# Performance work log

Hardware: AMD Instinct MI355X
Metric: run time of the kernel (lower is better)

The kernel has to match this reference:

```python
import jax, jax.numpy as jnp
import numpy as np

K = 3            # snake kernel size
MORPH = 0        # extend along depth axis
EXT = 1.0        # extend_scope
EPS = 1e-5
GROUPS = 16      # out_planes // 4


def conv3d(x, w, b, stride=(1, 1, 1), padding='SAME'):
    out = jax.lax.conv_general_dilated(
        x, w, window_strides=stride, padding=padding,
        dimension_numbers=('NCDHW', 'OIDHW', 'NCDHW'))
    return out + b[None, :, None, None, None]


def batchnorm(x, g, b):
    # training-mode BatchNorm3d (batch statistics, biased variance)
    m = x.mean(axis=(0, 2, 3, 4), keepdims=True)
    v = x.var(axis=(0, 2, 3, 4), keepdims=True)
    return (x - m) / jnp.sqrt(v + EPS) * g[None, :, None, None, None] + b[None, :, None, None, None]


def groupnorm(x, g, b):
    B, C, D, H, W = x.shape
    xg = x.reshape(B, GROUPS, C // GROUPS, D, H, W)
    m = xg.mean(axis=(2, 3, 4, 5), keepdims=True)
    v = xg.var(axis=(2, 3, 4, 5), keepdims=True)
    xn = ((xg - m) / jnp.sqrt(v + EPS)).reshape(B, C, D, H, W)
    return xn * g[None, :, None, None, None] + b[None, :, None, None, None]


def cumulative_offsets(off):
    # off: [B, K, D, H, W]; accumulate outward from kernel center (snake chaining)
    center = K // 2
    cums = [None] * K
    cums[center] = jnp.zeros_like(off[:, 0])
    for i in range(1, center + 1):
        cums[center + i] = cums[center + i - 1] + off[:, center + i]
        cums[center - i] = cums[center - i + 1] + off[:, center - i]
    return jnp.stack(cums, axis=1)  # [B, K, D, H, W]


def trilinear_sample_one(feat, z, y, x):
    # feat: [C, D, H, W]; z/y/x: [DK, H, W] float coords (already clamped)
    C, D, H, W = feat.shape
    z0f, y0f, x0f = jnp.floor(z), jnp.floor(y), jnp.floor(x)
    wz, wy, wx = z - z0f, y - y0f, x - x0f
    z0 = jnp.clip(z0f.astype(jnp.int32), 0, D - 1)
    y0 = jnp.clip(y0f.astype(jnp.int32), 0, H - 1)
    x0 = jnp.clip(x0f.astype(jnp.int32), 0, W - 1)
    z1 = jnp.clip(z0 + 1, 0, D - 1)
    y1 = jnp.clip(y0 + 1, 0, H - 1)
    x1 = jnp.clip(x0 + 1, 0, W - 1)

    def g(zi, yi, xi):
        return feat[:, zi, yi, xi]  # [C, DK, H, W]

    out = (g(z0, y0, x0) * ((1 - wz) * (1 - wy) * (1 - wx))[None]
         + g(z0, y0, x1) * ((1 - wz) * (1 - wy) * wx)[None]
         + g(z0, y1, x0) * ((1 - wz) * wy * (1 - wx))[None]
         + g(z0, y1, x1) * ((1 - wz) * wy * wx)[None]
         + g(z1, y0, x0) * (wz * (1 - wy) * (1 - wx))[None]
         + g(z1, y0, x1) * (wz * (1 - wy) * wx)[None]
         + g(z1, y1, x0) * (wz * wy * (1 - wx))[None]
         + g(z1, y1, x1) * (wz * wy * wx)[None])
    return out


def setup_inputs() -> dict:
    key = jax.random.key(0)
    ks = jax.random.split(key, 8)
    B, Cin, Cout, D, H, W = 2, 32, 64, 48, 48, 48
    x = jax.random.normal(ks[0], (B, Cin, D, H, W), dtype=jnp.float32)
    offset_w = jax.random.normal(ks[1], (3 * K, Cin, 3, 3, 3), dtype=jnp.float32) * 0.02
    offset_b = jnp.zeros((3 * K,), dtype=jnp.float32)
    bn_g = jnp.ones((3 * K,), dtype=jnp.float32)
    bn_b = jnp.zeros((3 * K,), dtype=jnp.float32)
    conv_w = jax.random.normal(ks[2], (Cout, Cin, K, 1, 1), dtype=jnp.float32) * 0.05
    conv_b = jnp.zeros((Cout,), dtype=jnp.float32)
    gn_g = jnp.ones((Cout,), dtype=jnp.float32)
    gn_b = jnp.zeros((Cout,), dtype=jnp.float32)
    return {"x": x, "offset_w": offset_w, "offset_b": offset_b, "bn_g": bn_g,
            "bn_b": bn_b, "conv_w": conv_w, "conv_b": conv_b, "gn_g": gn_g, "gn_b": gn_b}


def reference(x, offset_w, offset_b, bn_g, bn_b, conv_w, conv_b, gn_g, gn_b):
    B, C, D, H, W = x.shape
    dt = x.dtype
    # offset prediction: tanh(BN(conv3x3x3)) -> [B, 3K, D, H, W]
    off = jnp.tanh(batchnorm(conv3d(x, offset_w, offset_b), bn_g, bn_b))
    off_y = off[:, K:2 * K]   # perpendicular offsets (morph=0: H and W)
    off_x = off[:, 2 * K:]
    cy = cumulative_offsets(off_y)  # [B, K, D, H, W]
    cx = cumulative_offsets(off_x)
    center = K // 2
    kk = jnp.arange(K, dtype=dt) - center
    # coordinate maps [B, K, D, H, W]
    z = jnp.broadcast_to(jnp.arange(D, dtype=dt)[None, None, :, None, None]
                         + kk[None, :, None, None, None], (B, K, D, H, W))
    y = jnp.arange(H, dtype=dt)[None, None, None, :, None] + EXT * cy
    xc = jnp.arange(W, dtype=dt)[None, None, None, None, :] + EXT * cx
    z = jnp.clip(z, 0.0, D - 1)
    y = jnp.clip(y, 0.0, H - 1)
    xc = jnp.clip(xc, 0.0, W - 1)
    # interleave kernel points along depth: [B, D*K, H, W]
    il = lambda c: jnp.transpose(c, (0, 2, 1, 3, 4)).reshape(B, D * K, H, W)
    z, y, xc = il(z), il(y), il(xc)
    deformed = jax.vmap(trilinear_sample_one)(x, z, y, xc)  # [B, C, D*K, H, W]
    out = conv3d(deformed, conv_w, conv_b, stride=(K, 1, 1), padding='VALID')
    return jax.nn.relu(groupnorm(out, gn_g, gn_b))
```

## Files before the change

kernel.cpp:

```cpp
#include <hip/hip_runtime.h>
#include <hip/hip_bf16.h>

#define ZB    2
#define ZCIN  32
#define ZCOUT 64
#define ZD    48
#define ZH    48
#define ZW    48
#define ZHW   2304
#define ZDHW  110592
#define ZNPOS 221184
#define ZEPS  1e-5f

#define WFLAG    0
#define WCB      64
#define WBNSTAT  128
#define WGNSTAT  192
#define WBMAT    256
#define WBMATO   3328
#define WCONV    10240
#define WXTP     894976


template <int TAG>
__device__ __forceinline__ float ldT(const void* p, long i) {
    if (TAG == 1) return __bfloat162float(((const __hip_bfloat16*)p)[i]);
    return ((const float*)p)[i];
}

__device__ __forceinline__ unsigned short f2bu(float f) {
    unsigned int b = __float_as_uint(f);
    b += 0x7FFFu + ((b >> 16) & 1u);
    return (unsigned short)(b >> 16);
}
__device__ __forceinline__ float bu2f(unsigned short u) {
    return __uint_as_float(((unsigned int)u) << 16);
}

typedef short bf16x8 __attribute__((ext_vector_type(8)));
typedef float f32x4  __attribute__((ext_vector_type(4)));
typedef unsigned short u16x8 __attribute__((ext_vector_type(8)));

template <int TAG>
__device__ void begin_prep(const void* offset_w, const void* conv_w,
                           const void* conv_b, float* ws, int i) {
    if (i < 64) {
        ws[WCB + i] = ldT<TAG>(conv_b, i);
    } else if (i < 6208) {
        int j = i - 64;
        int n = j / 96, kk = j % 96;
        int kz = kk >> 5, ci = kk & 31;
        ((unsigned short*)(ws + WBMAT))[j] =
            f2bu(ldT<TAG>(conv_w, ((long)n * 32 + ci) * 3 + kz));
    } else if (i < 20032) {
        int j = i - 6208;
        int tap = j / 512, rem = j % 512;
        int n = rem >> 5, ci = rem & 31;
        float v = 0.f;
        if (n < 4) {
            int ch = (n == 0) ? 3 : (n == 1) ? 5 : (n == 2) ? 6 : 8;
            v = ldT<TAG>(offset_w, (long)ch * 864 + ci * 27 + tap);
        }
        ((unsigned short*)(ws + WBMATO))[j] = f2bu(v);
    } else if (i < 20160) {
        ws[WBNSTAT + (i - 20032)] = 0.0f;
    }
}

__device__ void begin_zero_boundary(float* ws, int v) {
    if (v >= 28816) return;
    int b = v / 14408, r = v % 14408;
    int z, y, x;
    if (r < 5000) {
        z = (r / 2500) * 49; int q = r % 2500; y = q / 50; x = q % 50;
    } else if (r < 9800) {
        int s = r - 5000; z = 1 + s / 100; int q = s % 100;
        y = (q / 50) * 49; x = q % 50;
    } else {
        int s = r - 9800; z = 1 + s / 96; int q = s % 96;
        y = 1 + q / 2; x = (q & 1) * 49;
    }
    unsigned short* xtp = (unsigned short*)(ws + WXTP);
    long base = ((((long)b * 50 + z) * 50 + y) * 50 + x) * 32;
    u16x8 zz = {0, 0, 0, 0, 0, 0, 0, 0};
#pragma unroll
    for (int k = 0; k < 4; ++k) *(u16x8*)&xtp[base + k * 8] = zz;
}

template <int TAG>
__device__ void begin_xpose(const void* x, float* ws, int bid2,
                            unsigned short* tile) {
    int b = bid2 / 2304, rem = bid2 % 2304;
    int z = rem / 48, y = rem % 48;
    int t = threadIdx.x;
    long ibase = (long)b * ZCIN * ZDHW + (long)z * ZHW + (long)y * ZW;
    if (TAG == 1) {
        if (t < 192) {
            int ci = t / 6, cb = t % 6;
            u16x8 v = *(const u16x8*)((const unsigned short*)x
                                      + ibase + (long)ci * ZDHW + cb * 8);
#pragma unroll
            for (int e = 0; e < 8; ++e)
                tile[(cb * 8 + e) * 34 + ci] = (unsigned short)v[e];
        }
    } else {
#pragma unroll
        for (int kk = 0; kk < 2; ++kk) {
            int c = t + kk * 256;
            if (c < 384) {
                int ci = c / 12, cb = c % 12;
                float4 v = *(const float4*)((const float*)x
                                            + ibase + (long)ci * ZDHW + cb * 4);
                tile[(cb * 4 + 0) * 34 + ci] = f2bu(v.x);
                tile[(cb * 4 + 1) * 34 + ci] = f2bu(v.y);
                tile[(cb * 4 + 2) * 34 + ci] = f2bu(v.z);
                tile[(cb * 4 + 3) * 34 + ci] = f2bu(v.w);
            }
        }
    }
    __syncthreads();
    long obase16 = ((((long)b * 50 + z + 1) * 50 + y + 1) * 50 + 1) * 32;
    unsigned int* o32 = (unsigned int*)((unsigned short*)(ws + WXTP) + obase16);
#pragma unroll
    for (int k = 0; k < 3; ++k) {
        int e2 = k * 256 + t;
        int xx = e2 >> 4, c2 = (e2 & 15) * 2;
        o32[e2] = (unsigned int)tile[xx * 34 + c2]
                | ((unsigned int)tile[xx * 34 + c2 + 1] << 16);
    }
}

__global__ void __launch_bounds__(256) zk_begin(const void* x, const void* offset_w,
                                                const void* conv_w, const void* conv_b,
                                                const unsigned short* bng, float* ws) {
    __shared__ unsigned short tile[48 * 34];
    int bid = blockIdx.x;
    bool isbf = (bng[0] != 0);
    if (bid < 79) {
        int i = bid * 256 + threadIdx.x;
        if (i == 0) ws[WFLAG] = isbf ? 1.0f : 2.0f;
        if (isbf) begin_prep<1>(offset_w, conv_w, conv_b, ws, i);
        else      begin_prep<2>(offset_w, conv_w, conv_b, ws, i);
    } else if (bid < 192) {
        begin_zero_boundary(ws, (bid - 79) * 256 + threadIdx.x);
    } else {
        if (isbf) begin_xpose<1>(x, ws, bid - 192, tile);
        else      begin_xpose<2>(x, ws, bid - 192, tile);
    }
}

__global__ void __launch_bounds__(256, 4) zk_offset_conv(float* ws) {
    const unsigned short* bmo = (const unsigned short*)(ws + WBMATO);
    const unsigned short* xtp = (const unsigned short*)(ws + WXTP);
    float* convout = ws + WCONV;

    __shared__ __align__(16) unsigned short slice[1280 * 8];
    __shared__ float sred[8];

    int t = threadIdx.x, lane = t & 63, wv = t >> 6;
    int quad = lane >> 4, col = lane & 15;
    int bid2 = (blockIdx.x & 7) * 144 + (blockIdx.x >> 3);
    int b  = bid2 / 576, rem = bid2 % 576;
    int z  = rem / 12, yt = rem % 12;
    int y0 = yt * 4;

    if (t < 8) sred[t] = 0.f;

    f32x4 acc[3];
#pragma unroll
    for (int mt = 0; mt < 3; ++mt) {
        acc[mt][0] = 0.f; acc[mt][1] = 0.f; acc[mt][2] = 0.f; acc[mt][3] = 0.f;
    }

#pragma unroll
    for (int kz = 0; kz < 3; ++kz) {
        long cb = (((long)b * 50 + (z + kz)) * 50 + y0) * 50 * 4;
        __syncthreads();
#pragma unroll
        for (int i = 0; i < 5; ++i) {
            int c = i * 256 + t;
            *(u16x8*)&slice[c * 8] = *(const u16x8*)&xtp[(cb + c) * 8];
        }
        __syncthreads();

        bf16x8 bfr[9];
#pragma unroll
        for (int j = 0; j < 9; ++j)
            bfr[j] = *(const bf16x8*)&bmo[((kz * 9 + j) * 16 + col) * 32 + quad * 8];

#pragma unroll
        for (int ky = 0; ky < 3; ++ky)
#pragma unroll
            for (int kx = 0; kx < 3; ++kx) {
                int j = ky * 3 + kx;
#pragma unroll
                for (int mt = 0; mt < 3; ++mt) {
                    int ch = ((wv + ky) * 50 + mt * 16 + col + kx) * 4 + quad;
                    bf16x8 a = *(const bf16x8*)&slice[ch * 8];
                    acc[mt] = __builtin_amdgcn_mfma_f32_16x16x32_bf16(
                                  a, bfr[j], acc[mt], 0, 0, 0);
                }
            }
    }

    float S = 0.f, Q = 0.f;
#pragma unroll
    for (int mt = 0; mt < 3; ++mt) {
        S += acc[mt][0] + acc[mt][1] + acc[mt][2] + acc[mt][3];
        Q += acc[mt][0] * acc[mt][0] + acc[mt][1] * acc[mt][1]
           + acc[mt][2] * acc[mt][2] + acc[mt][3] * acc[mt][3];
    }
    S += __shfl_xor(S, 16); S += __shfl_xor(S, 32);
    Q += __shfl_xor(Q, 16); Q += __shfl_xor(Q, 32);

    if (col < 4) {
        int rowbase = b * ZDHW + z * ZHW + (y0 + wv) * 48 + quad * 4;
#pragma unroll
        for (int mt = 0; mt < 3; ++mt)
            *(f32x4*)&convout[col * ZNPOS + rowbase + mt * 16] = acc[mt];
        if (quad == 0) {
            atomicAdd(&sred[col], S);
            atomicAdd(&sred[4 + col], Q);
        }
    }
    __syncthreads();
    if (t < 8) atomicAdd(&ws[WBNSTAT + t], sred[t]);
}

__device__ __forceinline__ void sample_plane(const unsigned short* xt,
        unsigned short* As, int tp, int kzslot, int b, int zp, int h, int w,
        float cy, float cx) {
    float fy = fminf(fmaxf((float)h + cy, 0.f), 47.f);
    float fx = fminf(fmaxf((float)w + cx, 0.f), 47.f);
    int y0 = (int)fy, x0 = (int)fx;
    float wy = fy - (float)y0, wx = fx - (float)x0;
    int y1 = (y0 < 47) ? y0 + 1 : 47, x1 = (x0 < 47) ? x0 + 1 : 47;
    long pb = ((long)b * 50 + zp + 1) * 50;
    long r0 = (pb + y0 + 1) * 50, r1 = (pb + y1 + 1) * 50;
    long a00 = (r0 + x0 + 1) * 32, a01 = (r0 + x1 + 1) * 32;
    long a10 = (r1 + x0 + 1) * 32, a11 = (r1 + x1 + 1) * 32;
    float u00 = (1.f - wy) * (1.f - wx), u01 = (1.f - wy) * wx;
    float u10 = wy * (1.f - wx),         u11 = wy * wx;
    u16x8 A[4], B[4], C[4], D[4];
#pragma unroll
    for (int j = 0; j < 4; ++j) {
        A[j] = *(const u16x8*)&xt[a00 + j * 8];
        B[j] = *(const u16x8*)&xt[a01 + j * 8];
        C[j] = *(const u16x8*)&xt[a10 + j * 8];
        D[j] = *(const u16x8*)&xt[a11 + j * 8];
    }
#pragma unroll
    for (int j = 0; j < 4; ++j) {
        u16x8 o;
#pragma unroll
        for (int e = 0; e < 8; ++e) {
            float v = u00 * bu2f((unsigned short)A[j][e])
                    + u01 * bu2f((unsigned short)B[j][e])
                    + u10 * bu2f((unsigned short)C[j][e])
                    + u11 * bu2f((unsigned short)D[j][e]);
            o[e] = f2bu(v);
        }
        *(u16x8*)&As[tp * 104 + kzslot * 32 + j * 8] = o;
    }
}

template <int TAG>
__device__ void deform_body(const void* bn_g, const void* bn_b,
                            float* ws, void* out,
                            unsigned short* As, float* sred) {
    const float* cb  = ws + WCB;
    const float* cvo = ws + WCONV;
    const unsigned short* bm = (const unsigned short*)(ws + WBMAT);
    const unsigned short* xt = (const unsigned short*)(ws + WXTP);
    float* gnstat = ws + WGNSTAT;

    int t    = threadIdx.x;
    int tp   = t & 255;
    int half = t >> 8;
    int bid  = blockIdx.x;
    int slab = (bid & 7) * 108 + (bid >> 3);
    int p    = slab * 256 + tp;
    int b    = p / ZDHW;
    int r    = p - b * ZDHW;
    int d = r / ZHW, r2 = r % ZHW;
    int h = r2 / ZW, w = r2 % ZW;

    if (t < 32) sred[t] = 0.f;

    float bnsc[4], bnsh[4];
#pragma unroll
    for (int c = 0; c < 4; ++c) {
        int ch = (c == 0) ? 3 : (c == 1) ? 5 : (c == 2) ? 6 : 8;
        float sum = ws[WBNSTAT + c], sq = ws[WBNSTAT + 4 + c];
        float mean = sum / (float)ZNPOS;
        float var  = sq / (float)ZNPOS - mean * mean;
        float inv  = rsqrtf(var + ZEPS);
        float g = ldT<TAG>(bn_g, ch), bb = ldT<TAG>(bn_b, ch);
        bnsc[c] = inv * g;
        bnsh[c] = bb - mean * inv * g;
    }

    if (half == 0) {
        float cy = tanhf(fmaf(cvo[p],             bnsc[0], bnsh[0]));
        float cx = tanhf(fmaf(cvo[2 * ZNPOS + p], bnsc[2], bnsh[2]));
        int zp = (d > 0) ? d - 1 : 0;
        sample_plane(xt, As, tp, 0, b, zp, h, w, cy, cx);
    } else {
        long base1 = ((((long)b * 50 + d + 1) * 50 + h + 1) * 50 + (w + 1)) * 32;
#pragma unroll
        for (int j = 0; j < 4; ++j)
            *(u16x8*)&As[tp * 104 + 32 + j * 8] = *(const u16x8*)&xt[base1 + j * 8];
        float cy = tanhf(fmaf(cvo[ZNPOS + p],     bnsc[1], bnsh[1]));
        float cx = tanhf(fmaf(cvo[3 * ZNPOS + p], bnsc[3], bnsh[3]));
        int zp = (d < ZD - 1) ? d + 1 : ZD - 1;
        sample_plane(xt, As, tp, 2, b, zp, h, w, cy, cx);
    }
    __syncthreads();

    int lane = t & 63, wv = t >> 6;
    int quad = lane >> 4, col = lane & 15;
    f32x4 acc[2][4];
#pragma unroll
    for (int nt = 0; nt < 4; ++nt) {
        float bias = cb[nt * 16 + col];
#pragma unroll
        for (int mt = 0; mt < 2; ++mt) {
            acc[mt][nt][0] = bias; acc[mt][nt][1] = bias;
            acc[mt][nt][2] = bias; acc[mt][nt][3] = bias;
        }
    }
#pragma unroll
    for (int kz = 0; kz < 3; ++kz) {
        bf16x8 bfr[4];
#pragma unroll
        for (int nt = 0; nt < 4; ++nt)
            bfr[nt] = *(const bf16x8*)&bm[(nt * 16 + col) * 96 + kz * 32 + quad * 8];
#pragma unroll
        for (int mt = 0; mt < 2; ++mt) {
            bf16x8 afr = *(const bf16x8*)&As[(32 * wv + 16 * mt + col) * 104
                                             + kz * 32 + quad * 8];
#pragma unroll
            for (int nt = 0; nt < 4; ++nt)
                acc[mt][nt] = __builtin_amdgcn_mfma_f32_16x16x32_bf16(
                                  afr, bfr[nt], acc[mt][nt], 0, 0, 0);
        }
    }

    int r0 = r - tp;
    long obase = (long)b * ZCOUT * ZDHW;
#pragma unroll
    for (int nt = 0; nt < 4; ++nt) {
        int co = nt * 16 + col;
        float S = 0.f, Q = 0.f;
        long cobase = obase + (long)co * ZDHW;
#pragma unroll
        for (int mt = 0; mt < 2; ++mt) {
            long rbase = cobase + r0 + 32 * wv + 16 * mt + quad * 4;
            f32x4 v = acc[mt][nt];
            S += v[0] + v[1] + v[2] + v[3];
            Q += v[0] * v[0] + v[1] * v[1] + v[2] * v[2] + v[3] * v[3];
            if (TAG == 2) {
                *(f32x4*)((float*)out + rbase) = v;
            } else {
                unsigned int lo = (unsigned int)f2bu(v[0]) | ((unsigned int)f2bu(v[1]) << 16);
                unsigned int hi = (unsigned int)f2bu(v[2]) | ((unsigned int)f2bu(v[3]) << 16);
                uint2 pk; pk.x = lo; pk.y = hi;
                *(uint2*)((__hip_bfloat16*)out + rbase) = pk;
            }
        }
        S += __shfl_xor(S, 16); S += __shfl_xor(S, 32);
        Q += __shfl_xor(Q, 16); Q += __shfl_xor(Q, 32);
        if (quad == 0) {
            int g = nt * 4 + (col >> 2);
            atomicAdd(&sred[g], S);
            atomicAdd(&sred[16 + g], Q);
        }
    }
    __syncthreads();
    if (t < 32) {
        int g = t & 15, isq = t >> 4;
        atomicAdd(&gnstat[isq * 32 + b * 16 + g], sred[t]);
    }
}

__global__ void __launch_bounds__(512, 4) zk_deform(const void* bn_g, const void* bn_b,
                                                    float* ws, void* out) {
    __shared__ __align__(16) unsigned short As[256 * 104];
    __shared__ float sred[32];
    if (ws[WFLAG] == 1.0f) deform_body<1>(bn_g, bn_b, ws, out, As, sred);
    else                   deform_body<2>(bn_g, bn_b, ws, out, As, sred);
}

template <int TAG>
__device__ void gn_body(void* out, const float* ws, const void* gn_g, const void* gn_b) {
    long i0 = ((long)blockIdx.x * 256 + threadIdx.x) * 8;
    int bc = (int)(i0 / ZDHW);
    int b = bc >> 6, co = bc & 63, g = co >> 2;
    float sum = ws[WGNSTAT + b * 16 + g];
    float sq  = ws[WGNSTAT + 32 + b * 16 + g];
    const float N = 4.0f * (float)ZDHW;
    float mean = sum / N;
    float var  = sq / N - mean * mean;
    float inv  = rsqrtf(var + ZEPS);
    float gg = ldT<TAG>(gn_g, co), gb = ldT<TAG>(gn_b, co);
    float scale = inv * gg;
    float shift = gb - mean * inv * gg;

    if (TAG == 1) {
        u16x8* vp = (u16x8*)((__hip_bfloat16*)out + i0);
        u16x8 v = *vp;
#pragma unroll
        for (int j = 0; j < 8; ++j) {
            float f = bu2f((unsigned short)v[j]);
            f = fmaxf(fmaf(f, scale, shift), 0.f);
            v[j] = f2bu(f);
        }
        *vp = v;
    } else {
        float4* op = (float4*)((float*)out + i0);
        float4 v0 = op[0], v1 = op[1];
        v0.x = fmaxf(fmaf(v0.x, scale, shift), 0.f);
        v0.y = fmaxf(fmaf(v0.y, scale, shift), 0.f);
        v0.z = fmaxf(fmaf(v0.z, scale, shift), 0.f);
        v0.w = fmaxf(fmaf(v0.w, scale, shift), 0.f);
        v1.x = fmaxf(fmaf(v1.x, scale, shift), 0.f);
        v1.y = fmaxf(fmaf(v1.y, scale, shift), 0.f);
        v1.z = fmaxf(fmaf(v1.z, scale, shift), 0.f);
        v1.w = fmaxf(fmaf(v1.w, scale, shift), 0.f);
        op[0] = v0; op[1] = v1;
    }
}

__global__ void __launch_bounds__(256) zk_gn_apply(void* out, const float* ws,
                                                   const void* gn_g, const void* gn_b) {
    if (ws[WFLAG] == 1.0f) gn_body<1>(out, ws, gn_g, gn_b);
    else                   gn_body<2>(out, ws, gn_g, gn_b);
}

extern "C" void kernel_launch(void* const* d_in, const int* in_sizes, int n_in,
                              void* d_out, int out_size, void* d_ws, size_t ws_size,
                              hipStream_t stream) {
    const void* x        = d_in[0];
    const void* offset_w = d_in[1];
    const void* bn_g     = d_in[3];
    const void* bn_b     = d_in[4];
    const void* conv_w   = d_in[5];
    const void* conv_b   = d_in[6];
    const void* gn_g     = d_in[7];
    const void* gn_b     = d_in[8];
    float* ws = (float*)d_ws;

    zk_begin<<<4800, 256, 0, stream>>>(x, offset_w, conv_w, conv_b,
                                       (const unsigned short*)bn_g, ws);

    zk_offset_conv<<<1152, 256, 0, stream>>>(ws);

    zk_deform<<<864, 512, 0, stream>>>(bn_g, bn_b, ws, d_out);

    int ngn = out_size / 8 / 256;
    zk_gn_apply<<<ngn, 256, 0, stream>>>(d_out, ws, gn_g, gn_b);
}
```

Before: 173.5 us.

## Stage sampled depth planes in shared memory and split deform into per-kz passes

```diff
diff --git a/kernel.cpp b/kernel.cpp
--- a/kernel.cpp
+++ b/kernel.cpp
@@ -120,13 +120,13 @@
     }
     __syncthreads();
     long obase16 = ((((long)b * 50 + z + 1) * 50 + y + 1) * 50 + 1) * 32;
-    unsigned int* o32 = (unsigned int*)((unsigned short*)(ws + WXTP) + obase16);
-#pragma unroll
-    for (int k = 0; k < 3; ++k) {
-        int e2 = k * 256 + t;
-        int xx = e2 >> 4, c2 = (e2 & 15) * 2;
-        o32[e2] = (unsigned int)tile[xx * 34 + c2]
-                | ((unsigned int)tile[xx * 34 + c2 + 1] << 16);
+    unsigned short* op = (unsigned short*)(ws + WXTP) + obase16;
+    if (t < 192) {
+        int xx = t >> 2, c8 = (t & 3) * 8;
+        u16x8 o;
+#pragma unroll
+        for (int e = 0; e < 8; ++e) o[e] = tile[xx * 34 + c8 + e];
+        *(u16x8*)(op + xx * 32 + c8) = o;
     }
 }
 
@@ -227,47 +227,11 @@
     if (t < 8) atomicAdd(&ws[WBNSTAT + t], sred[t]);
 }
 
-__device__ __forceinline__ void sample_plane(const unsigned short* xt,
-        unsigned short* As, int tp, int kzslot, int b, int zp, int h, int w,
-        float cy, float cx) {
-    float fy = fminf(fmaxf((float)h + cy, 0.f), 47.f);
-    float fx = fminf(fmaxf((float)w + cx, 0.f), 47.f);
-    int y0 = (int)fy, x0 = (int)fx;
-    float wy = fy - (float)y0, wx = fx - (float)x0;
-    int y1 = (y0 < 47) ? y0 + 1 : 47, x1 = (x0 < 47) ? x0 + 1 : 47;
-    long pb = ((long)b * 50 + zp + 1) * 50;
-    long r0 = (pb + y0 + 1) * 50, r1 = (pb + y1 + 1) * 50;
-    long a00 = (r0 + x0 + 1) * 32, a01 = (r0 + x1 + 1) * 32;
-    long a10 = (r1 + x0 + 1) * 32, a11 = (r1 + x1 + 1) * 32;
-    float u00 = (1.f - wy) * (1.f - wx), u01 = (1.f - wy) * wx;
-    float u10 = wy * (1.f - wx),         u11 = wy * wx;
-    u16x8 A[4], B[4], C[4], D[4];
-#pragma unroll
-    for (int j = 0; j < 4; ++j) {
-        A[j] = *(const u16x8*)&xt[a00 + j * 8];
-        B[j] = *(const u16x8*)&xt[a01 + j * 8];
-        C[j] = *(const u16x8*)&xt[a10 + j * 8];
-        D[j] = *(const u16x8*)&xt[a11 + j * 8];
-    }
-#pragma unroll
-    for (int j = 0; j < 4; ++j) {
-        u16x8 o;
-#pragma unroll
-        for (int e = 0; e < 8; ++e) {
-            float v = u00 * bu2f((unsigned short)A[j][e])
-                    + u01 * bu2f((unsigned short)B[j][e])
-                    + u10 * bu2f((unsigned short)C[j][e])
-                    + u11 * bu2f((unsigned short)D[j][e]);
-            o[e] = f2bu(v);
-        }
-        *(u16x8*)&As[tp * 104 + kzslot * 32 + j * 8] = o;
-    }
-}
-
 template <int TAG>
 __device__ void deform_body(const void* bn_g, const void* bn_b,
                             float* ws, void* out,
-                            unsigned short* As, float* sred) {
+                            unsigned short* plane, unsigned short* As,
+                            float* sred) {
     const float* cb  = ws + WCB;
     const float* cvo = ws + WCONV;
     const unsigned short* bm = (const unsigned short*)(ws + WBMAT);
@@ -276,14 +240,18 @@
 
     int t    = threadIdx.x;
     int tp   = t & 255;
-    int half = t >> 8;
+    int jp   = t >> 8;
     int bid  = blockIdx.x;
     int slab = (bid & 7) * 108 + (bid >> 3);
-    int p    = slab * 256 + tp;
-    int b    = p / ZDHW;
-    int r    = p - b * ZDHW;
-    int d = r / ZHW, r2 = r % ZHW;
-    int h = r2 / ZW, w = r2 % ZW;
+    int p0   = slab * 256;
+    int b    = p0 / ZDHW;
+    int r0   = p0 - b * ZDHW;
+    int d    = r0 / ZHW;
+    int s9   = (r0 % ZHW) >> 8;
+    int ylo  = (s9 * 256) / 48;
+    int r2   = s9 * 256 + tp;
+    int h    = r2 / 48, w = r2 % 48;
+    int p    = p0 + tp;
 
     if (t < 32) sred[t] = 0.f;
 
@@ -300,23 +268,6 @@
         bnsh[c] = bb - mean * inv * g;
     }
 
-    if (half == 0) {
-        float cy = tanhf(fmaf(cvo[p],             bnsc[0], bnsh[0]));
-        float cx = tanhf(fmaf(cvo[2 * ZNPOS + p], bnsc[2], bnsh[2]));
-        int zp = (d > 0) ? d - 1 : 0;
-        sample_plane(xt, As, tp, 0, b, zp, h, w, cy, cx);
-    } else {
-        long base1 = ((((long)b * 50 + d + 1) * 50 + h + 1) * 50 + (w + 1)) * 32;
-#pragma unroll
-        for (int j = 0; j < 4; ++j)
-            *(u16x8*)&As[tp * 104 + 32 + j * 8] = *(const u16x8*)&xt[base1 + j * 8];
-        float cy = tanhf(fmaf(cvo[ZNPOS + p],     bnsc[1], bnsh[1]));
-        float cx = tanhf(fmaf(cvo[3 * ZNPOS + p], bnsc[3], bnsh[3]));
-        int zp = (d < ZD - 1) ? d + 1 : ZD - 1;
-        sample_plane(xt, As, tp, 2, b, zp, h, w, cy, cx);
-    }
-    __syncthreads();
-
     int lane = t & 63, wv = t >> 6;
     int quad = lane >> 4, col = lane & 15;
     f32x4 acc[2][4];
@@ -329,24 +280,157 @@
             acc[mt][nt][2] = bias; acc[mt][nt][3] = bias;
         }
     }
-#pragma unroll
-    for (int kz = 0; kz < 3; ++kz) {
+
+    int zpad0 = ((d > 0) ? d - 1 : 0) + 1;
+    int zpad2 = ((d < ZD - 1) ? d + 1 : ZD - 1) + 1;
+
+    {
+        long gc = ((long)(b * 50 + zpad0) * 50 + ylo) * 50 * 4;
+#pragma unroll
+        for (int i = 0; i < 4; ++i) {
+            int c = i * 512 + t;
+            if (c < 1800)
+                *(u16x8*)&plane[c * 8] = *(const u16x8*)&xt[(gc + c) * 8];
+        }
+    }
+    __syncthreads();
+
+    {
+        float cy = tanhf(fmaf(cvo[p],             bnsc[0], bnsh[0]));
+        float cx = tanhf(fmaf(cvo[2 * ZNPOS + p], bnsc[2], bnsh[2]));
+        float fy = fminf(fmaxf((float)h + cy, 0.f), 47.f);
+        float fx = fminf(fmaxf((float)w + cx, 0.f), 47.f);
+        int y0 = (int)fy, x0 = (int)fx;
+        float wy = fy - (float)y0, wx = fx - (float)x0;
+        int y1 = (y0 < 47) ? y0 + 1 : 47, x1 = (x0 < 47) ? x0 + 1 : 47;
+        int cA = ((y0 + 1 - ylo) * 50 + x0 + 1) * 4;
+        int cB = ((y0 + 1 - ylo) * 50 + x1 + 1) * 4;
+        int cC = ((y1 + 1 - ylo) * 50 + x0 + 1) * 4;
+        int cD = ((y1 + 1 - ylo) * 50 + x1 + 1) * 4;
+        float u00 = (1.f - wy) * (1.f - wx), u01 = (1.f - wy) * wx;
+        float u10 = wy * (1.f - wx),         u11 = wy * wx;
+#pragma unroll
+        for (int q = 0; q < 2; ++q) {
+            int jj = jp * 2 + q;
+            u16x8 A = *(const u16x8*)&plane[(cA + jj) * 8];
+            u16x8 B = *(const u16x8*)&plane[(cB + jj) * 8];
+            u16x8 C = *(const u16x8*)&plane[(cC + jj) * 8];
+            u16x8 D = *(const u16x8*)&plane[(cD + jj) * 8];
+            u16x8 o;
+#pragma unroll
+            for (int e = 0; e < 8; ++e) {
+                float v = u00 * bu2f((unsigned short)A[e])
+                        + u01 * bu2f((unsigned short)B[e])
+                        + u10 * bu2f((unsigned short)C[e])
+                        + u11 * bu2f((unsigned short)D[e]);
+                o[e] = f2bu(v);
+            }
+            *(u16x8*)&As[(tp * 5 + jj) * 8] = o;
+        }
+    }
+    __syncthreads();
+
+    {
         bf16x8 bfr[4];
 #pragma unroll
         for (int nt = 0; nt < 4; ++nt)
-            bfr[nt] = *(const bf16x8*)&bm[(nt * 16 + col) * 96 + kz * 32 + quad * 8];
+            bfr[nt] = *(const bf16x8*)&bm[(nt * 16 + col) * 96 + 0 * 32 + quad * 8];
 #pragma unroll
         for (int mt = 0; mt < 2; ++mt) {
-            bf16x8 afr = *(const bf16x8*)&As[(32 * wv + 16 * mt + col) * 104
-                                             + kz * 32 + quad * 8];
+            bf16x8 afr = *(const bf16x8*)&As[(32 * wv + 16 * mt + col) * 40 + quad * 8];
 #pragma unroll
             for (int nt = 0; nt < 4; ++nt)
                 acc[mt][nt] = __builtin_amdgcn_mfma_f32_16x16x32_bf16(
                                   afr, bfr[nt], acc[mt][nt], 0, 0, 0);
         }
-    }
-
-    int r0 = r - tp;
+        long gc = ((long)(b * 50 + zpad2) * 50 + ylo) * 50 * 4;
+#pragma unroll
+        for (int i = 0; i < 4; ++i) {
+            int c = i * 512 + t;
+            if (c < 1800)
+                *(u16x8*)&plane[c * 8] = *(const u16x8*)&xt[(gc + c) * 8];
+        }
+    }
+    __syncthreads();
+
+    {
+        float cy = tanhf(fmaf(cvo[ZNPOS + p],     bnsc[1], bnsh[1]));
+        float cx = tanhf(fmaf(cvo[3 * ZNPOS + p], bnsc[3], bnsh[3]));
+        float fy = fminf(fmaxf((float)h + cy, 0.f), 47.f);
+        float fx = fminf(fmaxf((float)w + cx, 0.f), 47.f);
+        int y0 = (int)fy, x0 = (int)fx;
+        float wy = fy - (float)y0, wx = fx - (float)x0;
+        int y1 = (y0 < 47) ? y0 + 1 : 47, x1 = (x0 < 47) ? x0 + 1 : 47;
+        int cA = ((y0 + 1 - ylo) * 50 + x0 + 1) * 4;
+        int cB = ((y0 + 1 - ylo) * 50 + x1 + 1) * 4;
+        int cC = ((y1 + 1 - ylo) * 50 + x0 + 1) * 4;
+        int cD = ((y1 + 1 - ylo) * 50 + x1 + 1) * 4;
+        float u00 = (1.f - wy) * (1.f - wx), u01 = (1.f - wy) * wx;
+        float u10 = wy * (1.f - wx),         u11 = wy * wx;
+#pragma unroll
+        for (int q = 0; q < 2; ++q) {
+            int jj = jp * 2 + q;
+            u16x8 A = *(const u16x8*)&plane[(cA + jj) * 8];
+            u16x8 B = *(const u16x8*)&plane[(cB + jj) * 8];
+            u16x8 C = *(const u16x8*)&plane[(cC + jj) * 8];
+            u16x8 D = *(const u16x8*)&plane[(cD + jj) * 8];
+            u16x8 o;
+#pragma unroll
+            for (int e = 0; e < 8; ++e) {
+                float v = u00 * bu2f((unsigned short)A[e])
+                        + u01 * bu2f((unsigned short)B[e])
+                        + u10 * bu2f((unsigned short)C[e])
+                        + u11 * bu2f((unsigned short)D[e]);
+                o[e] = f2bu(v);
+            }
+            *(u16x8*)&As[(tp * 5 + jj) * 8] = o;
+        }
+    }
+    __syncthreads();
+
+    {
+        bf16x8 bfr[4];
+#pragma unroll
+        for (int nt = 0; nt < 4; ++nt)
+            bfr[nt] = *(const bf16x8*)&bm[(nt * 16 + col) * 96 + 2 * 32 + quad * 8];
+#pragma unroll
+        for (int mt = 0; mt < 2; ++mt) {
+            bf16x8 afr = *(const bf16x8*)&As[(32 * wv + 16 * mt + col) * 40 + quad * 8];
+#pragma unroll
+            for (int nt = 0; nt < 4; ++nt)
+                acc[mt][nt] = __builtin_amdgcn_mfma_f32_16x16x32_bf16(
+                                  afr, bfr[nt], acc[mt][nt], 0, 0, 0);
+        }
+    }
+    __syncthreads();
+
+#pragma unroll
+    for (int i = 0; i < 2; ++i) {
+        int c = i * 512 + t;
+        int pos = c >> 2, jj = c & 3;
+        int rr = s9 * 256 + pos;
+        int h1 = rr / 48, w1 = rr % 48;
+        long g = (((long)(b * 50 + d + 1) * 50 + h1 + 1) * 50 + w1 + 1) * 4 + jj;
+        *(u16x8*)&As[(pos * 5 + jj) * 8] = *(const u16x8*)&xt[g * 8];
+    }
+    __syncthreads();
+
+    {
+        bf16x8 bfr[4];
+#pragma unroll
+        for (int nt = 0; nt < 4; ++nt)
+            bfr[nt] = *(const bf16x8*)&bm[(nt * 16 + col) * 96 + 1 * 32 + quad * 8];
+#pragma unroll
+        for (int mt = 0; mt < 2; ++mt) {
+            bf16x8 afr = *(const bf16x8*)&As[(32 * wv + 16 * mt + col) * 40 + quad * 8];
+#pragma unroll
+            for (int nt = 0; nt < 4; ++nt)
+                acc[mt][nt] = __builtin_amdgcn_mfma_f32_16x16x32_bf16(
+                                  afr, bfr[nt], acc[mt][nt], 0, 0, 0);
+        }
+    }
+
+    int r0g = p - b * ZDHW - tp;
     long obase = (long)b * ZCOUT * ZDHW;
 #pragma unroll
     for (int nt = 0; nt < 4; ++nt) {
@@ -355,7 +439,7 @@
         long cobase = obase + (long)co * ZDHW;
 #pragma unroll
         for (int mt = 0; mt < 2; ++mt) {
-            long rbase = cobase + r0 + 32 * wv + 16 * mt + quad * 4;
+            long rbase = cobase + r0g + 32 * wv + 16 * mt + quad * 4;
             f32x4 v = acc[mt][nt];
             S += v[0] + v[1] + v[2] + v[3];
             Q += v[0] * v[0] + v[1] * v[1] + v[2] * v[2] + v[3] * v[3];
@@ -385,17 +469,20 @@
 
 __global__ void __launch_bounds__(512, 4) zk_deform(const void* bn_g, const void* bn_b,
                                                     float* ws, void* out) {
-    __shared__ __align__(16) unsigned short As[256 * 104];
+    __shared__ __align__(16) unsigned short plane[1800 * 8];
+    __shared__ __align__(16) unsigned short As[256 * 40];
     __shared__ float sred[32];
-    if (ws[WFLAG] == 1.0f) deform_body<1>(bn_g, bn_b, ws, out, As, sred);
-    else                   deform_body<2>(bn_g, bn_b, ws, out, As, sred);
+    if (ws[WFLAG] == 1.0f) deform_body<1>(bn_g, bn_b, ws, out, plane, As, sred);
+    else                   deform_body<2>(bn_g, bn_b, ws, out, plane, As, sred);
 }
 
 template <int TAG>
 __device__ void gn_body(void* out, const float* ws, const void* gn_g, const void* gn_b) {
-    long i0 = ((long)blockIdx.x * 256 + threadIdx.x) * 8;
-    int bc = (int)(i0 / ZDHW);
-    int b = bc >> 6, co = bc & 63, g = co >> 2;
+    int t = threadIdx.x, bid = blockIdx.x;
+    int k = bid & 7, j = bid >> 3;
+    int b = k >> 2, rc = k & 3;
+    int co = j / 27, cc = j % 27;
+    int g = co >> 2;
     float sum = ws[WGNSTAT + b * 16 + g];
     float sq  = ws[WGNSTAT + 32 + b * 16 + g];
     const float N = 4.0f * (float)ZDHW;
@@ -406,14 +493,16 @@
     float scale = inv * gg;
     float shift = gb - mean * inv * gg;
 
+    long i0 = ((long)(b * 64 + co)) * ZDHW + rc * 27648 + cc * 1024 + t * 8;
+
     if (TAG == 1) {
         u16x8* vp = (u16x8*)((__hip_bfloat16*)out + i0);
         u16x8 v = *vp;
 #pragma unroll
-        for (int j = 0; j < 8; ++j) {
-            float f = bu2f((unsigned short)v[j]);
+        for (int jj = 0; jj < 8; ++jj) {
+            float f = bu2f((unsigned short)v[jj]);
             f = fmaxf(fmaf(f, scale, shift), 0.f);
-            v[j] = f2bu(f);
+            v[jj] = f2bu(f);
         }
         *vp = v;
     } else {
@@ -431,7 +520,7 @@
     }
 }
 
-__global__ void __launch_bounds__(256) zk_gn_apply(void* out, const float* ws,
+__global__ void __launch_bounds__(128) zk_gn_apply(void* out, const float* ws,
                                                    const void* gn_g, const void* gn_b) {
     if (ws[WFLAG] == 1.0f) gn_body<1>(out, ws, gn_g, gn_b);
     else                   gn_body<2>(out, ws, gn_g, gn_b);
@@ -457,6 +546,5 @@
 
     zk_deform<<<864, 512, 0, stream>>>(bn_g, bn_b, ws, d_out);
 
-    int ngn = out_size / 8 / 256;
-    zk_gn_apply<<<ngn, 256, 0, stream>>>(d_out, ws, gn_g, gn_b);
-}
+    zk_gn_apply<<<13824, 128, 0, stream>>>(d_out, ws, gn_g, gn_b);
+}
```

Result: slower. 179.0 us (+3.2%).
